# Optimization experiments

Measured on AMD Instinct MI355X. Metric: run time of the kernel, lower is better.

The kernel has to match this reference:

```python
import jax, jax.numpy as jnp
import numpy as np

TEMPERATURE = 0.1
NORM_EPS = 1e-12          # F.normalize default eps
SMALL_VAL = float(np.finfo(np.float32).tiny)  # pytorch-metric-learning small_val(float32)
NEG_INF = float(np.finfo(np.float32).min)     # c_f.neg_inf for masked logsumexp


def setup_inputs() -> dict:
    key = jax.random.key(0)
    k1, k2 = jax.random.split(key)
    N, D = 8192, 128
    emb = jax.random.normal(k1, (N, D), dtype=jnp.float32)
    labels = jax.random.randint(k2, (N,), 0, 1000, dtype=jnp.int64)
    return {"emb": emb, "labels": labels}


def reference(emb, labels):
    N = emb.shape[0]
    # F.normalize(emb, dim=1): x / max(||x||, eps)
    norms = jnp.linalg.norm(emb, axis=1, keepdims=True)
    x = emb / jnp.maximum(norms, NORM_EPS)

    # cosine similarity matrix [N, N], scaled by temperature
    mat = jnp.matmul(x, x.T) / TEMPERATURE

    same = labels[:, None] == labels[None, :]
    diag = jnp.eye(N, dtype=bool)
    pos_mask = same & ~diag          # same label, i != j
    keep_mask = ~diag                # pos + neg (all off-diagonal)

    # numerical stability: subtract detached row max (over full row, incl. diagonal)
    mat_max = jax.lax.stop_gradient(jnp.max(mat, axis=1, keepdims=True))
    mat = mat - mat_max

    # masked logsumexp over off-diagonal entries
    masked = jnp.where(keep_mask, mat, NEG_INF)
    denom = jax.nn.logsumexp(masked, axis=1, keepdims=True)  # [N, 1]

    log_prob = mat - denom
    pos_f = pos_mask.astype(mat.dtype)
    mean_log_prob_pos = jnp.sum(pos_f * log_prob, axis=1) / (
        jnp.sum(pos_f, axis=1) + SMALL_VAL
    )
    losses = -mean_log_prob_pos  # per-element losses
    # SumReducer: sum over elements
    return jnp.sum(losses)
```

## Files before the change

kernel.cpp:

```cpp
#include <hip/hip_runtime.h>
#include <hip/hip_bf16.h>


typedef __bf16 bf16_t;
typedef __bf16 bf16x2 __attribute__((ext_vector_type(2)));
typedef __bf16 bf16x8 __attribute__((ext_vector_type(8)));
typedef float f32x16 __attribute__((ext_vector_type(16)));

#define NN 8192
#define DIM 128
#define SWEEP 16
#define SMALL_VAL 1.17549435e-38f
#define L2E10 14.4269504089f
#define LN2 0.69314718056f

__device__ inline size_t swz(int row, int lane) {
    int f = lane >> 3, hh = (lane >> 2) & 1, j = (lane & 3) << 1;
    return ((size_t)(row >> 5) * 4096) + f * 512 + hh * 256 + (row & 31) * 8 + j;
}

#define DPPADD(v, ctrl, rmask)                                                         \
    do {                                                                               \
        int _t = __builtin_amdgcn_update_dpp(0, __float_as_int((v)), (ctrl), (rmask),  \
                                             0xf, true);                               \
        (v) += __int_as_float(_t);                                                     \
    } while (0)

__device__ inline float half32_sum(float v) {
    DPPADD(v, 0x111, 0xf);
    DPPADD(v, 0x112, 0xf);
    DPPADD(v, 0x114, 0xf);
    DPPADD(v, 0x118, 0xf);
    DPPADD(v, 0x142, 0xa);
    return v;
}

__device__ inline void gload_lds16(const bf16_t* g, bf16_t* l) {
    __builtin_amdgcn_global_load_lds(
        (const __attribute__((address_space(1))) unsigned int*)g,
        (__attribute__((address_space(3))) unsigned int*)l, 16, 0, 0);
}

__global__ __launch_bounds__(256) void norm_csum(const float* __restrict__ emb,
                                                 const int* __restrict__ labels,
                                                 bf16_t* __restrict__ xsw,
                                                 float* __restrict__ cd_arr,
                                                 float* __restrict__ sd_arr,
                                                 float* __restrict__ cm1_arr,
                                                 float* __restrict__ out) {
    __shared__ float cs[DIM];
    __shared__ int rowlist[96];
    __shared__ int nrows;
    int cls = blockIdx.x;
    int wv = threadIdx.x >> 6, lane = threadIdx.x & 63;
    if (threadIdx.x < DIM) cs[threadIdx.x] = 0.f;
    if (threadIdx.x == 0) nrows = 0;
    if (cls == 0 && threadIdx.x == 0) *out = 0.f;
    __syncthreads();

    float s0 = 0.f, s1 = 0.f;
    const int4* lab4 = (const int4*)(labels + wv * 2048);
#pragma unroll
    for (int it = 0; it < 8; ++it) {
        int4 l = lab4[it * 64 + lane];
        int base = wv * 2048 + it * 256;
#pragma unroll
        for (int cmp = 0; cmp < 4; ++cmp) {
            int li = (cmp == 0) ? l.x : (cmp == 1) ? l.y : (cmp == 2) ? l.z : l.w;
            unsigned long long m = __ballot(li == cls);
            while (m) {
                int bb = __builtin_ctzll(m);
                m &= m - 1;
                int row = base + 4 * bb + cmp;
                float2 v = ((const float2*)emb)[row * 64 + lane];
                float ss = fmaf(v.x, v.x, v.y * v.y);
#pragma unroll
                for (int mm = 1; mm < 64; mm <<= 1) ss += __shfl_xor(ss, mm, 64);
                float inv = 1.0f / fmaxf(sqrtf(ss), 1e-12f);
                bf16x2 o; o.x = (bf16_t)(v.x * inv); o.y = (bf16_t)(v.y * inv);
                *(bf16x2*)(xsw + swz(row, lane)) = o;
                s0 += (float)o.x; s1 += (float)o.y;
                if (lane == 0) {
                    int idx = atomicAdd(&nrows, 1);
                    if (idx < 96) rowlist[idx] = row;
                }
            }
        }
    }
    atomicAdd(&cs[2 * lane], s0);
    atomicAdd(&cs[2 * lane + 1], s1);
    __syncthreads();
    int n = nrows;
    for (int k = wv; k < n; k += 4) {
        int row = rowlist[k];
        bf16x2 xv = *(const bf16x2*)(xsw + swz(row, lane));
        float x0 = (float)xv.x, x1 = (float)xv.y;
        float cdp = fmaf(x0, cs[2 * lane], x1 * cs[2 * lane + 1]);
        float sdp = fmaf(x0, x0, x1 * x1);
#pragma unroll
        for (int mm = 1; mm < 64; mm <<= 1) {
            cdp += __shfl_xor(cdp, mm, 64);
            sdp += __shfl_xor(sdp, mm, 64);
        }
        if (lane == 0) {
            cd_arr[row] = cdp; sd_arr[row] = sdp; cm1_arr[row] = (float)(n - 1);
        }
    }
}

__global__
__attribute__((amdgpu_flat_work_group_size(256, 256)))
__attribute__((amdgpu_waves_per_eu(2, 2)))
void supcon_sweep(const bf16_t* __restrict__ xsw,
                  float* __restrict__ se_part) {
    __shared__ bf16_t bst[2][4 * 4096];

    int s = blockIdx.x & 15, rb = blockIdx.x >> 4;
    int wv = threadIdx.x >> 6, lane = threadIdx.x & 63;
    int I = rb * 4 + wv;
    int c = lane & 31, h = lane >> 5;
    int laneoff = h * 256 + c * 8;

    const bf16_t* abase = xsw + (size_t)I * 4096 + laneoff;
    bf16x8 a[8];
#pragma unroll
    for (int f = 0; f < 8; ++f) a[f] = *(const bf16x8*)(abase + f * 512);

    float se[16];
#pragma unroll
    for (int r = 0; r < 16; ++r) se[r] = 0.f;

    {
        const bf16_t* gsrc = xsw + (size_t)s * 16384;
#pragma unroll
        for (int i = 0; i < 8; ++i) {
            int kk = i * 4 + wv;
            gload_lds16(gsrc + kk * 512 + lane * 8, &bst[0][kk * 512]);
        }
    }
    __syncthreads();

#pragma unroll 1
    for (int k = 0; k < 4; ++k) {
        if (k < 3) {
            const bf16_t* gsrc = xsw + (size_t)(s + 16 * (k + 1)) * 16384;
            bf16_t* dbuf = &bst[(k + 1) & 1][0];
#pragma unroll
            for (int i = 0; i < 8; ++i) {
                int kk = i * 4 + wv;
                gload_lds16(gsrc + kk * 512 + lane * 8, dbuf + kk * 512);
            }
        }
        const bf16_t* bb = &bst[k & 1][0];

#pragma unroll
        for (int t = 0; t < 4; ++t) {
            f32x16 acc;
#pragma unroll
            for (int r = 0; r < 16; ++r) acc[r] = 0.f;
            const bf16_t* bt = bb + t * 4096 + laneoff;
#pragma unroll
            for (int f = 0; f < 8; ++f) {
                bf16x8 bfr = *(const bf16x8*)(bt + f * 512);
                acc = __builtin_amdgcn_mfma_f32_32x32x16_bf16(a[f], bfr, acc, 0, 0, 0);
            }
#pragma unroll
            for (int r = 0; r < 16; ++r)
                se[r] += __builtin_amdgcn_exp2f(fmaf(acc[r], L2E10, -L2E10));
        }
        __syncthreads();
    }

#pragma unroll
    for (int r = 0; r < 16; ++r) se[r] = half32_sum(se[r]);
    if (c == 31) {
        float* dst = se_part + (size_t)s * NN + I * 32 + 4 * h;
#pragma unroll
        for (int r = 0; r < 16; ++r)
            dst[(r & 3) + 8 * (r >> 2)] = se[r];
    }
}

__global__ __launch_bounds__(256) void finalize_kernel(const float* __restrict__ se_part,
                                                       const float* __restrict__ cd_arr,
                                                       const float* __restrict__ sd_arr,
                                                       const float* __restrict__ cm1_arr,
                                                       float* __restrict__ out) {
    __shared__ float part[4];
    int i = blockIdx.x * 256 + threadIdx.x;
    float sev_raw = 0.f;
#pragma unroll
    for (int s = 0; s < SWEEP; ++s) sev_raw += se_part[(size_t)s * NN + i];
    float sd = sd_arr[i], cd = cd_arr[i], cm1 = cm1_arr[i];
    float diag = __builtin_amdgcn_exp2f(fmaf(sd, L2E10, -L2E10));
    float sev  = fmaxf(sev_raw - diag, 1e-30f);
    float lse  = fmaf(__builtin_amdgcn_logf(sev), LN2, 10.f);
    float loss = (cm1 * lse - 10.f * (cd - sd)) / (cm1 + SMALL_VAL);
#pragma unroll
    for (int m = 1; m < 64; m <<= 1) loss += __shfl_xor(loss, m, 64);
    int wv = threadIdx.x >> 6;
    if ((threadIdx.x & 63) == 0) part[wv] = loss;
    __syncthreads();
    if (threadIdx.x == 0) atomicAdd(out, part[0] + part[1] + part[2] + part[3]);
}

extern "C" void kernel_launch(void* const* d_in, const int* in_sizes, int n_in,
                              void* d_out, int out_size, void* d_ws, size_t ws_size,
                              hipStream_t stream) {
    const float* emb  = (const float*)d_in[0];
    const int* labels = (const int*)d_in[1];

    char* ws = (char*)d_ws;
    bf16_t* xsw   = (bf16_t*)ws;
    float* separt = (float*)(ws + (size_t)NN * DIM * 2);
    float* cd     = separt + (size_t)SWEEP * NN;
    float* sd     = cd + NN;
    float* cm1    = sd + NN;

    norm_csum<<<1024, 256, 0, stream>>>(emb, labels, xsw, cd, sd, cm1, (float*)d_out);
    supcon_sweep<<<1024, 256, 0, stream>>>(xsw, separt);
    finalize_kernel<<<NN / 256, 256, 0, stream>>>(separt, cd, sd, cm1, (float*)d_out);
}
```

Measured before the change: 93.64 us.

## Replace per-class label scan with per-row normalize and atomic class sums

The normalization kernel no longer has each of the 1024 class blocks scan all 8192 labels. It now normalizes one row per wave and accumulates per-class centroid sums and counts with global atomics into a memset-cleared buffer. The per-row positive dot products move into the finalize kernel, which reads each row, its class sum and the sweep partials and reduces them with shuffles. This removes the redundant label scan but adds a memset launch, heavy global float atomics and more work in finalize.

Result: slower. 104.6 us (+11.7%).

```diff
diff --git a/kernel.cpp b/kernel.cpp
--- a/kernel.cpp
+++ b/kernel.cpp
@@ -10,6 +10,7 @@
 #define NN 8192
 #define DIM 128
 #define SWEEP 16
+#define NCLS 1024
 #define SMALL_VAL 1.17549435e-38f
 #define L2E10 14.4269504089f
 #define LN2 0.69314718056f
@@ -41,71 +42,28 @@
         (__attribute__((address_space(3))) unsigned int*)l, 16, 0, 0);
 }
 
-__global__ __launch_bounds__(256) void norm_csum(const float* __restrict__ emb,
+__global__ __launch_bounds__(256) void norm_rows(const float* __restrict__ emb,
                                                  const int* __restrict__ labels,
                                                  bf16_t* __restrict__ xsw,
-                                                 float* __restrict__ cd_arr,
-                                                 float* __restrict__ sd_arr,
-                                                 float* __restrict__ cm1_arr,
+                                                 float* __restrict__ csum,
+                                                 int* __restrict__ count,
                                                  float* __restrict__ out) {
-    __shared__ float cs[DIM];
-    __shared__ int rowlist[96];
-    __shared__ int nrows;
-    int cls = blockIdx.x;
     int wv = threadIdx.x >> 6, lane = threadIdx.x & 63;
-    if (threadIdx.x < DIM) cs[threadIdx.x] = 0.f;
-    if (threadIdx.x == 0) nrows = 0;
-    if (cls == 0 && threadIdx.x == 0) *out = 0.f;
-    __syncthreads();
+    int row = blockIdx.x * 4 + wv;
+    if (blockIdx.x == 0 && threadIdx.x == 0) *out = 0.f;
 
-    float s0 = 0.f, s1 = 0.f;
-    const int4* lab4 = (const int4*)(labels + wv * 2048);
+    float2 v = ((const float2*)emb)[row * 64 + lane];
+    float ss = fmaf(v.x, v.x, v.y * v.y);
 #pragma unroll
-    for (int it = 0; it < 8; ++it) {
-        int4 l = lab4[it * 64 + lane];
-        int base = wv * 2048 + it * 256;
-#pragma unroll
-        for (int cmp = 0; cmp < 4; ++cmp) {
-            int li = (cmp == 0) ? l.x : (cmp == 1) ? l.y : (cmp == 2) ? l.z : l.w;
-            unsigned long long m = __ballot(li == cls);
-            while (m) {
-                int bb = __builtin_ctzll(m);
-                m &= m - 1;
-                int row = base + 4 * bb + cmp;
-                float2 v = ((const float2*)emb)[row * 64 + lane];
-                float ss = fmaf(v.x, v.x, v.y * v.y);
-#pragma unroll
-                for (int mm = 1; mm < 64; mm <<= 1) ss += __shfl_xor(ss, mm, 64);
-                float inv = 1.0f / fmaxf(sqrtf(ss), 1e-12f);
-                bf16x2 o; o.x = (bf16_t)(v.x * inv); o.y = (bf16_t)(v.y * inv);
-                *(bf16x2*)(xsw + swz(row, lane)) = o;
-                s0 += (float)o.x; s1 += (float)o.y;
-                if (lane == 0) {
-                    int idx = atomicAdd(&nrows, 1);
-                    if (idx < 96) rowlist[idx] = row;
-                }
-            }
-        }
-    }
-    atomicAdd(&cs[2 * lane], s0);
-    atomicAdd(&cs[2 * lane + 1], s1);
-    __syncthreads();
-    int n = nrows;
-    for (int k = wv; k < n; k += 4) {
-        int row = rowlist[k];
-        bf16x2 xv = *(const bf16x2*)(xsw + swz(row, lane));
-        float x0 = (float)xv.x, x1 = (float)xv.y;
-        float cdp = fmaf(x0, cs[2 * lane], x1 * cs[2 * lane + 1]);
-        float sdp = fmaf(x0, x0, x1 * x1);
-#pragma unroll
-        for (int mm = 1; mm < 64; mm <<= 1) {
-            cdp += __shfl_xor(cdp, mm, 64);
-            sdp += __shfl_xor(sdp, mm, 64);
-        }
-        if (lane == 0) {
-            cd_arr[row] = cdp; sd_arr[row] = sdp; cm1_arr[row] = (float)(n - 1);
-        }
-    }
+    for (int m = 1; m < 64; m <<= 1) ss += __shfl_xor(ss, m, 64);
+    float inv = 1.0f / fmaxf(sqrtf(ss), 1e-12f);
+    bf16x2 o; o.x = (bf16_t)(v.x * inv); o.y = (bf16_t)(v.y * inv);
+    *(bf16x2*)(xsw + swz(row, lane)) = o;
+
+    int lab = labels[row];
+    atomicAdd(&csum[lab * DIM + 2 * lane],     (float)o.x);
+    atomicAdd(&csum[lab * DIM + 2 * lane + 1], (float)o.y);
+    if (lane == 0) atomicAdd(&count[lab], 1);
 }
 
 __global__
@@ -181,27 +139,44 @@
     }
 }
 
-__global__ __launch_bounds__(256) void finalize_kernel(const float* __restrict__ se_part,
-                                                       const float* __restrict__ cd_arr,
-                                                       const float* __restrict__ sd_arr,
-                                                       const float* __restrict__ cm1_arr,
-                                                       float* __restrict__ out) {
-    __shared__ float part[4];
-    int i = blockIdx.x * 256 + threadIdx.x;
-    float sev_raw = 0.f;
+__global__ __launch_bounds__(512) void finalize2(const bf16_t* __restrict__ xsw,
+                                                 const float* __restrict__ se_part,
+                                                 const float* __restrict__ csum,
+                                                 const int* __restrict__ count,
+                                                 const int* __restrict__ labels,
+                                                 float* __restrict__ out) {
+    __shared__ float part[8];
+    int wv = threadIdx.x >> 6, lane = threadIdx.x & 63;
+    int i = blockIdx.x * 8 + wv;
+
+    int lab = labels[i];
+    bf16x2 xv = *(const bf16x2*)(xsw + swz(i, lane));
+    float x0 = (float)xv.x, x1 = (float)xv.y;
+    float2 cs2 = *(const float2*)(csum + lab * DIM + 2 * lane);
+    float sp = (lane < SWEEP) ? se_part[(size_t)lane * NN + i] : 0.f;
+
+    float cdp = fmaf(x0, cs2.x, x1 * cs2.y);
+    float sdp = fmaf(x0, x0, x1 * x1);
 #pragma unroll
-    for (int s = 0; s < SWEEP; ++s) sev_raw += se_part[(size_t)s * NN + i];
-    float sd = sd_arr[i], cd = cd_arr[i], cm1 = cm1_arr[i];
-    float diag = __builtin_amdgcn_exp2f(fmaf(sd, L2E10, -L2E10));
-    float sev  = fmaxf(sev_raw - diag, 1e-30f);
-    float lse  = fmaf(__builtin_amdgcn_logf(sev), LN2, 10.f);
-    float loss = (cm1 * lse - 10.f * (cd - sd)) / (cm1 + SMALL_VAL);
+    for (int m = 1; m < 64; m <<= 1) {
+        cdp += __shfl_xor(cdp, m, 64);
+        sdp += __shfl_xor(sdp, m, 64);
+        sp  += __shfl_xor(sp,  m, 64);
+    }
+    if (lane == 0) {
+        float cm1  = (float)(count[lab] - 1);
+        float diag = __builtin_amdgcn_exp2f(fmaf(sdp, L2E10, -L2E10));
+        float sev  = fmaxf(sp - diag, 1e-30f);
+        float lse  = fmaf(__builtin_amdgcn_logf(sev), LN2, 10.f);
+        part[wv] = (cm1 * lse - 10.f * (cdp - sdp)) / (cm1 + SMALL_VAL);
+    }
+    __syncthreads();
+    if (threadIdx.x == 0) {
+        float t = 0.f;
 #pragma unroll
-    for (int m = 1; m < 64; m <<= 1) loss += __shfl_xor(loss, m, 64);
-    int wv = threadIdx.x >> 6;
-    if ((threadIdx.x & 63) == 0) part[wv] = loss;
-    __syncthreads();
-    if (threadIdx.x == 0) atomicAdd(out, part[0] + part[1] + part[2] + part[3]);
+        for (int w = 0; w < 8; ++w) t += part[w];
+        atomicAdd(out, t);
+    }
 }
 
 extern "C" void kernel_launch(void* const* d_in, const int* in_sizes, int n_in,
@@ -213,11 +188,11 @@
     char* ws = (char*)d_ws;
     bf16_t* xsw   = (bf16_t*)ws;
     float* separt = (float*)(ws + (size_t)NN * DIM * 2);
-    float* cd     = separt + (size_t)SWEEP * NN;
-    float* sd     = cd + NN;
-    float* cm1    = sd + NN;
+    float* csum   = separt + (size_t)SWEEP * NN;
+    int*   count  = (int*)(csum + (size_t)NCLS * DIM);
 
-    norm_csum<<<1024, 256, 0, stream>>>(emb, labels, xsw, cd, sd, cm1, (float*)d_out);
+    hipMemsetAsync(csum, 0, ((size_t)NCLS * DIM + NCLS) * sizeof(float), stream);
+    norm_rows<<<NN / 4, 256, 0, stream>>>(emb, labels, xsw, csum, count, (float*)d_out);
     supcon_sweep<<<1024, 256, 0, stream>>>(xsw, separt);
-    finalize_kernel<<<NN / 256, 256, 0, stream>>>(separt, cd, sd, cm1, (float*)d_out);
+    finalize2<<<NN / 8, 512, 0, stream>>>(xsw, separt, csum, count, labels, (float*)d_out);
 }
```

## Exploit symmetry of similarity matrix to compute only upper-triangle tiles

Applied to the files above, without the earlier changes.

Because the cosine similarity matrix is symmetric, the sweep kernel now computes each off-diagonal 128x128 block pair once. It accumulates the exponentials both into row sums and into column sums, which are written to a new column-partial buffer. The block count is halved, and the finalize kernel also sums up to 128 column partials per row. This cuts the MFMA and exp work roughly in half, at the cost of extra shuffles, global stores and a heavier finalize reduction.

Result: slower. 97.28 us (+3.9%).

```diff
diff --git a/kernel.cpp b/kernel.cpp
--- a/kernel.cpp
+++ b/kernel.cpp
@@ -9,7 +9,6 @@
 
 #define NN 8192
 #define DIM 128
-#define SWEEP 16
 #define SMALL_VAL 1.17549435e-38f
 #define L2E10 14.4269504089f
 #define LN2 0.69314718056f
@@ -111,15 +110,17 @@
 __global__
 __attribute__((amdgpu_flat_work_group_size(256, 256)))
 __attribute__((amdgpu_waves_per_eu(2, 2)))
-void supcon_sweep(const bf16_t* __restrict__ xsw,
-                  float* __restrict__ se_part) {
+void supcon_tri(const bf16_t* __restrict__ xsw,
+                float* __restrict__ rowpart,
+                float* __restrict__ colW) {
     __shared__ bf16_t bst[2][4 * 4096];
 
-    int s = blockIdx.x & 15, rb = blockIdx.x >> 4;
+    int p = blockIdx.x & 7, r = blockIdx.x >> 3;
     int wv = threadIdx.x >> 6, lane = threadIdx.x & 63;
-    int I = rb * 4 + wv;
-    int c = lane & 31, h = lane >> 5;
-    int laneoff = h * 256 + c * 8;
+    int I = r * 4 + wv;
+    int c32 = lane & 31, h = lane >> 5;
+    int laneoff = h * 256 + c32 * 8;
+    int nd = 4 + ((p == 0 && r < 32) ? 1 : 0);
 
     const bf16_t* abase = xsw + (size_t)I * 4096 + laneoff;
     bf16x8 a[8];
@@ -128,10 +129,10 @@
 
     float se[16];
 #pragma unroll
-    for (int r = 0; r < 16; ++r) se[r] = 0.f;
+    for (int rr = 0; rr < 16; ++rr) se[rr] = 0.f;
 
     {
-        const bf16_t* gsrc = xsw + (size_t)s * 16384;
+        const bf16_t* gsrc = xsw + (size_t)(((r + p) & 63)) * 16384;
 #pragma unroll
         for (int i = 0; i < 8; ++i) {
             int kk = i * 4 + wv;
@@ -141,56 +142,81 @@
     __syncthreads();
 
 #pragma unroll 1
-    for (int k = 0; k < 4; ++k) {
-        if (k < 3) {
-            const bf16_t* gsrc = xsw + (size_t)(s + 16 * (k + 1)) * 16384;
-            bf16_t* dbuf = &bst[(k + 1) & 1][0];
+    for (int ki = 0; ki < nd; ++ki) {
+        int d = (ki < 4) ? (p + 8 * ki) : 32;
+        int cc = (r + d) & 63;
+        if (ki + 1 < nd) {
+            int dn = (ki + 1 < 4) ? (p + 8 * (ki + 1)) : 32;
+            const bf16_t* gsrc = xsw + (size_t)((r + dn) & 63) * 16384;
+            bf16_t* dbuf = &bst[(ki + 1) & 1][0];
 #pragma unroll
             for (int i = 0; i < 8; ++i) {
                 int kk = i * 4 + wv;
                 gload_lds16(gsrc + kk * 512 + lane * 8, dbuf + kk * 512);
             }
         }
-        const bf16_t* bb = &bst[k & 1][0];
-
+        const bf16_t* bb = &bst[ki & 1][0];
+
+        float colsum[4];
 #pragma unroll
         for (int t = 0; t < 4; ++t) {
             f32x16 acc;
 #pragma unroll
-            for (int r = 0; r < 16; ++r) acc[r] = 0.f;
+            for (int rr = 0; rr < 16; ++rr) acc[rr] = 0.f;
             const bf16_t* bt = bb + t * 4096 + laneoff;
 #pragma unroll
             for (int f = 0; f < 8; ++f) {
                 bf16x8 bfr = *(const bf16x8*)(bt + f * 512);
                 acc = __builtin_amdgcn_mfma_f32_32x32x16_bf16(a[f], bfr, acc, 0, 0, 0);
             }
-#pragma unroll
-            for (int r = 0; r < 16; ++r)
-                se[r] += __builtin_amdgcn_exp2f(fmaf(acc[r], L2E10, -L2E10));
+            float cst = 0.f;
+#pragma unroll
+            for (int rr = 0; rr < 16; ++rr) {
+                float e = __builtin_amdgcn_exp2f(fmaf(acc[rr], L2E10, -L2E10));
+                se[rr] += e;
+                cst += e;
+            }
+            colsum[t] = cst;
+        }
+        if (d != 0) {
+#pragma unroll
+            for (int t = 0; t < 4; ++t) {
+                float v = colsum[t] + __shfl_xor(colsum[t], 32, 64);
+                if (h == 0)
+                    colW[(size_t)(((d - 1) << 2) + wv) * NN + cc * 128 + t * 32 + c32] = v;
+            }
         }
         __syncthreads();
     }
 
 #pragma unroll
-    for (int r = 0; r < 16; ++r) se[r] = half32_sum(se[r]);
-    if (c == 31) {
-        float* dst = se_part + (size_t)s * NN + I * 32 + 4 * h;
-#pragma unroll
-        for (int r = 0; r < 16; ++r)
-            dst[(r & 3) + 8 * (r >> 2)] = se[r];
-    }
-}
-
-__global__ __launch_bounds__(256) void finalize_kernel(const float* __restrict__ se_part,
-                                                       const float* __restrict__ cd_arr,
-                                                       const float* __restrict__ sd_arr,
-                                                       const float* __restrict__ cm1_arr,
-                                                       float* __restrict__ out) {
+    for (int rr = 0; rr < 16; ++rr) se[rr] = half32_sum(se[rr]);
+    if (c32 == 31) {
+        float* dst = rowpart + (size_t)p * NN + I * 32 + 4 * h;
+#pragma unroll
+        for (int rr = 0; rr < 16; ++rr)
+            dst[(rr & 3) + 8 * (rr >> 2)] = se[rr];
+    }
+}
+
+__global__ __launch_bounds__(256) void finalize_tri(const float* __restrict__ rowpart,
+                                                    const float* __restrict__ colW,
+                                                    const float* __restrict__ cd_arr,
+                                                    const float* __restrict__ sd_arr,
+                                                    const float* __restrict__ cm1_arr,
+                                                    float* __restrict__ out) {
     __shared__ float part[4];
     int i = blockIdx.x * 256 + threadIdx.x;
     float sev_raw = 0.f;
 #pragma unroll
-    for (int s = 0; s < SWEEP; ++s) sev_raw += se_part[(size_t)s * NN + i];
+    for (int pp = 0; pp < 8; ++pp) sev_raw += rowpart[(size_t)pp * NN + i];
+    int lim = (i >= 4096) ? 128 : 124;
+#pragma unroll 4
+    for (int j = 0; j < 124; ++j) sev_raw += colW[(size_t)j * NN + i];
+    if (lim == 128) {
+#pragma unroll
+        for (int j = 124; j < 128; ++j) sev_raw += colW[(size_t)j * NN + i];
+    }
     float sd = sd_arr[i], cd = cd_arr[i], cm1 = cm1_arr[i];
     float diag = __builtin_amdgcn_exp2f(fmaf(sd, L2E10, -L2E10));
     float sev  = fmaxf(sev_raw - diag, 1e-30f);
@@ -211,13 +237,14 @@
     const int* labels = (const int*)d_in[1];
 
     char* ws = (char*)d_ws;
-    bf16_t* xsw   = (bf16_t*)ws;
-    float* separt = (float*)(ws + (size_t)NN * DIM * 2);
-    float* cd     = separt + (size_t)SWEEP * NN;
-    float* sd     = cd + NN;
-    float* cm1    = sd + NN;
+    bf16_t* xsw    = (bf16_t*)ws;
+    float* rowpart = (float*)(ws + (size_t)NN * DIM * 2);
+    float* colW    = rowpart + (size_t)8 * NN;
+    float* cd      = colW + (size_t)128 * NN;
+    float* sd      = cd + NN;
+    float* cm1     = sd + NN;
 
     norm_csum<<<1024, 256, 0, stream>>>(emb, labels, xsw, cd, sd, cm1, (float*)d_out);
-    supcon_sweep<<<1024, 256, 0, stream>>>(xsw, separt);
-    finalize_kernel<<<NN / 256, 256, 0, stream>>>(separt, cd, sd, cm1, (float*)d_out);
-}
+    supcon_tri<<<512, 256, 0, stream>>>(xsw, rowpart, colW);
+    finalize_tri<<<NN / 256, 256, 0, stream>>>(rowpart, colW, cd, sd, cm1, (float*)d_out);
+}
```
